# Kernel tuning notes

Measured on AMD Instinct MI355X. Metric: run time of the kernel, lower is better.

The kernel has to match this reference:

```python
import jax, jax.numpy as jnp
import numpy as np

B, N, C = 8, 2049, 768
H, NB = 12, 4
HD = C // H          # 64
SPB = (N - 1) // NB  # 512
SCALE = HD ** -0.5
EPS = 1e-6


def layer_norm(x, w, b):
    mu = jnp.mean(x, axis=-1, keepdims=True)
    var = jnp.mean((x - mu) ** 2, axis=-1, keepdims=True)
    return (x - mu) * jax.lax.rsqrt(var + EPS) * w + b


def setup_inputs() -> dict:
    key = jax.random.key(0)
    ks = jax.random.split(key, 6)
    s = lambda fan_in: 1.0 / np.sqrt(fan_in)
    return {
        "x": jax.random.normal(ks[0], (B, N, C), jnp.float32),
        "ln1_w": jnp.ones((C,), jnp.float32),
        "ln1_b": jnp.zeros((C,), jnp.float32),
        "qkv_w": jax.random.normal(ks[1], (3 * C, C), jnp.float32) * s(C),
        "proj_w": jax.random.normal(ks[2], (C, C), jnp.float32) * s(C),
        "proj_b": jnp.zeros((C,), jnp.float32),
        "ln2_w": jnp.ones((C,), jnp.float32),
        "ln2_b": jnp.zeros((C,), jnp.float32),
        "fc1_w": jax.random.normal(ks[3], (4 * C, C), jnp.float32) * s(C),
        "fc1_b": jnp.zeros((4 * C,), jnp.float32),
        "fc2_w": jax.random.normal(ks[4], (C, 4 * C), jnp.float32) * s(4 * C),
        "fc2_b": jnp.zeros((C,), jnp.float32),
    }


def _sdpa(q, k, v):
    # q:[...,Q,D] k,v:[...,K,D]
    scores = jnp.einsum("...qd,...kd->...qk", q, k) * SCALE
    return jnp.einsum("...qk,...kd->...qd", jax.nn.softmax(scores, axis=-1), v)


def _attention(h, qkv_w, proj_w, proj_b):
    # h: [B,N,C] (already layer-normed)
    qkv = (h @ qkv_w.T).reshape(B, N, 3, H, HD).transpose(2, 0, 3, 1, 4)  # [3,B,H,N,HD]
    q, k, v = qkv[0], qkv[1], qkv[2]

    # cls token attends globally over all N keys
    cls_att = _sdpa(q[:, :, 0:1, :], k, v)            # [B,H,1,HD]
    cls = cls_att.reshape(B, 1, C) + h[:, 0:1, :]      # benign reshape (seq=1)

    qkv_c = (cls @ qkv_w.T).reshape(B, 1, 3, H, HD).transpose(2, 0, 3, 1, 4)  # [3,B,H,1,HD]
    qc, kc, vc = qkv_c[0], qkv_c[1], qkv_c[2]

    # per-branch local attention with shared cls kv prepended
    def branch(t, tc):
        tb = t[:, :, 1:, :].reshape(B, H, NB, SPB, HD)
        tcb = jnp.broadcast_to(tc[:, :, None, :, :], (B, H, NB, 1, HD))
        return jnp.concatenate([tcb, tb], axis=3)      # [B,H,NB,SPB+1,HD]

    out = _sdpa(branch(q, qc), branch(k, kc), branch(v, vc))[:, :, :, 1:, :]  # [B,H,NB,SPB,HD]
    # faithful replication of the source's reshape((B, spb, C)) on a [B,H,spb,HD]
    # tensor WITHOUT head transpose (raw row-major reinterpretation):
    out = out.transpose(0, 2, 1, 3, 4).reshape(B, NB, SPB, C).reshape(B, NB * SPB, C)

    y = jnp.concatenate([cls, out], axis=1)            # [B,N,C]
    return y @ proj_w.T + proj_b


def reference(x, ln1_w, ln1_b, qkv_w, proj_w, proj_b, ln2_w, ln2_b, fc1_w, fc1_b, fc2_w, fc2_b):
    x = x + _attention(layer_norm(x, ln1_w, ln1_b), qkv_w, proj_w, proj_b)
    h = layer_norm(x, ln2_w, ln2_b)
    h = jax.nn.gelu(h @ fc1_w.T + fc1_b, approximate=False) @ fc2_w.T + fc2_b
    return x + h
```

## Files before the change

kernel.cpp:

```cpp
#include <hip/hip_runtime.h>
#include <hip/hip_bf16.h>

typedef unsigned short u16;
typedef __attribute__((ext_vector_type(8))) short s16x8;
typedef __attribute__((ext_vector_type(4))) float f32x4;

#define MFMA16 __builtin_amdgcn_mfma_f32_16x16x32_bf16
#define AS1 __attribute__((address_space(1)))
#define AS3 __attribute__((address_space(3)))

__device__ __forceinline__ u16 f2bf(float f) {
    union { __hip_bfloat16 h; u16 u; } cv;
    cv.h = __float2bfloat16(f);
    return cv.u;
}
__device__ __forceinline__ float bf2f(u16 u) {
    unsigned int v = ((unsigned int)u) << 16;
    return __uint_as_float(v);
}
__device__ __forceinline__ void gll16(const u16* g, u16* l) {
    __builtin_amdgcn_global_load_lds((AS1 void*)g, (AS3 void*)l, 16, 0, 0);
}

__global__ void cvt_kernel(const float* __restrict__ src, u16* __restrict__ dst, int n) {
    int i = (blockIdx.x * 256 + threadIdx.x) * 4;
    if (i + 3 < n) {
        float4 v = *(const float4*)&src[i];
        u16 o0 = f2bf(v.x), o1 = f2bf(v.y), o2 = f2bf(v.z), o3 = f2bf(v.w);
        ushort4 o; o.x = o0; o.y = o1; o.z = o2; o.w = o3;
        *(ushort4*)&dst[i] = o;
    }
}

__global__ __launch_bounds__(256) void ln_kernel(const float* __restrict__ x,
                                                 const float* __restrict__ w,
                                                 const float* __restrict__ b,
                                                 u16* __restrict__ out) {
    int tok = blockIdx.x;
    int tid = threadIdx.x;
    const float* xr = x + (size_t)tok * 768;
    float v0 = xr[tid], v1 = xr[tid + 256], v2 = xr[tid + 512];
    float s = v0 + v1 + v2;
    float s2 = v0 * v0 + v1 * v1 + v2 * v2;
    #pragma unroll
    for (int d = 1; d < 64; d <<= 1) { s += __shfl_xor(s, d); s2 += __shfl_xor(s2, d); }
    __shared__ float red[8];
    int wv = tid >> 6, l = tid & 63;
    if (l == 0) { red[wv] = s; red[4 + wv] = s2; }
    __syncthreads();
    s = red[0] + red[1] + red[2] + red[3];
    s2 = red[4] + red[5] + red[6] + red[7];
    float mu = s * (1.0f / 768.0f);
    float var = s2 * (1.0f / 768.0f) - mu * mu;
    float rs = rsqrtf(var + 1e-6f);
    u16* orow = out + (size_t)tok * 768;
    orow[tid]       = f2bf((v0 - mu) * rs * w[tid]       + b[tid]);
    orow[tid + 256] = f2bf((v1 - mu) * rs * w[tid + 256] + b[tid + 256]);
    orow[tid + 512] = f2bf((v2 - mu) * rs * w[tid + 512] + b[tid + 512]);
}

template<int EPI>
__global__ __launch_bounds__(256, 2) void gemm_bt(const u16* __restrict__ A,
                                                  const u16* __restrict__ Bw,
                                                  const float* __restrict__ bias,
                                                  const float* __restrict__ res,
                                                  float* __restrict__ outF,
                                                  u16* __restrict__ outU,
                                                  int M, int N, int K) {
    __shared__ u16 lds[8192];
    const int tid = threadIdx.x;
    const int l = tid & 63, w = tid >> 6;
    const int wm = w >> 1, wn = w & 1;
    const int g = l >> 4, c = l & 15;
    const int m0 = blockIdx.y * 128, n0 = blockIdx.x * 128;

    f32x4 zf = {0.f, 0.f, 0.f, 0.f};
    f32x4 acc[4][4];
    #pragma unroll
    for (int m = 0; m < 4; ++m)
        #pragma unroll
        for (int n = 0; n < 4; ++n) acc[m][n] = zf;

    const u16* aS[2]; const u16* bS[2];
    #pragma unroll
    for (int iss = 0; iss < 2; ++iss) {
        int fs = iss * 256 + tid;
        int r = fs >> 2;
        int gk = (fs & 3) ^ ((r >> 1) & 3);
        int ra = m0 + r; if (ra > M - 1) ra = M - 1;
        aS[iss] = A + (size_t)ra * K + gk * 8;
        bS[iss] = Bw + (size_t)(n0 + r) * K + gk * 8;
    }
    u16* aD0 = &lds[(0   + w * 64) * 8];
    u16* aD1 = &lds[(256 + w * 64) * 8];
    u16* bD0 = &lds[4096 + (0   + w * 64) * 8];
    u16* bD1 = &lds[4096 + (256 + w * 64) * 8];

    int aoff[4], boff[4];
    #pragma unroll
    for (int m = 0; m < 4; ++m) {
        int r = wm * 64 + m * 16 + c;
        aoff[m] = r * 32 + ((g ^ ((r >> 1) & 3)) * 8);
        int rb = wn * 64 + m * 16 + c;
        boff[m] = 4096 + rb * 32 + ((g ^ ((rb >> 1) & 3)) * 8);
    }

    for (int k0 = 0; k0 < K; k0 += 32) {
        gll16(aS[0] + k0, aD0);
        gll16(aS[1] + k0, aD1);
        gll16(bS[0] + k0, bD0);
        gll16(bS[1] + k0, bD1);
        __syncthreads();
        s16x8 af[4], bfr[4];
        #pragma unroll
        for (int m = 0; m < 4; ++m) af[m] = *(const s16x8*)&lds[aoff[m]];
        #pragma unroll
        for (int n = 0; n < 4; ++n) bfr[n] = *(const s16x8*)&lds[boff[n]];
        #pragma unroll
        for (int m = 0; m < 4; ++m)
            #pragma unroll
            for (int n = 0; n < 4; ++n)
                acc[m][n] = MFMA16(af[m], bfr[n], acc[m][n], 0, 0, 0);
        __syncthreads();
    }

    #pragma unroll
    for (int n = 0; n < 4; ++n) {
        int col = n0 + wn * 64 + n * 16 + c;
        float bv = (EPI >= 1) ? bias[col] : 0.0f;
        #pragma unroll
        for (int m = 0; m < 4; ++m) {
            int rowb = m0 + wm * 64 + m * 16 + g * 4;
            #pragma unroll
            for (int j = 0; j < 4; ++j) {
                int row = rowb + j;
                if (row < M) {
                    float v = acc[m][n][j];
                    size_t idx = (size_t)row * N + col;
                    if (EPI == 0) {
                        outU[idx] = f2bf(v);
                    } else if (EPI == 1) {
                        outF[idx] = res[idx] + v + bv;
                    } else {
                        float t = v + bv;
                        t = 0.5f * t * (1.0f + erff(t * 0.70710678118654752f));
                        outU[idx] = f2bf(t);
                    }
                }
            }
        }
    }
}

__global__ __launch_bounds__(256) void cls_part(const u16* __restrict__ qkv,
                                                float* __restrict__ part) {
    int bid = blockIdx.x;
    int ch = bid % 17;
    int hh = (bid / 17) % 12;
    int b = bid / (17 * 12);
    int tid = threadIdx.x, l = tid & 63, w = tid >> 6;
    size_t base = (size_t)b * 2049 * 2304;
    float qv = bf2f(qkv[base + hh * 64 + l]);
    __shared__ float sc[128];
    __shared__ float red[8];
    __shared__ float pv[4][64];
    int j0 = ch * 128;
    int nk = 2049 - j0; if (nk > 128) nk = 128;

    for (int jj = w; jj < nk; jj += 4) {
        float kv = bf2f(qkv[base + (size_t)(j0 + jj) * 2304 + 768 + hh * 64 + l]);
        float p = qv * kv;
        p += __shfl_xor(p, 1);  p += __shfl_xor(p, 2);  p += __shfl_xor(p, 4);
        p += __shfl_xor(p, 8);  p += __shfl_xor(p, 16); p += __shfl_xor(p, 32);
        if (l == 0) sc[jj] = p * 0.125f;
    }
    __syncthreads();
    float mx = -1e30f;
    for (int jj = tid; jj < nk; jj += 256) mx = fmaxf(mx, sc[jj]);
    #pragma unroll
    for (int d = 1; d < 64; d <<= 1) mx = fmaxf(mx, __shfl_xor(mx, d));
    if (l == 0) red[w] = mx;
    __syncthreads();
    mx = fmaxf(fmaxf(red[0], red[1]), fmaxf(red[2], red[3]));
    float sum = 0.0f;
    for (int jj = tid; jj < nk; jj += 256) {
        float p = __expf(sc[jj] - mx);
        sc[jj] = p;
        sum += p;
    }
    #pragma unroll
    for (int d = 1; d < 64; d <<= 1) sum += __shfl_xor(sum, d);
    if (l == 0) red[4 + w] = sum;
    __syncthreads();
    sum = red[4] + red[5] + red[6] + red[7];

    float acc = 0.0f;
    for (int jj = w; jj < nk; jj += 4)
        acc += sc[jj] * bf2f(qkv[base + (size_t)(j0 + jj) * 2304 + 1536 + hh * 64 + l]);
    pv[w][l] = acc;
    __syncthreads();
    if (tid < 64) {
        float o = pv[0][tid] + pv[1][tid] + pv[2][tid] + pv[3][tid];
        float* rec = part + ((size_t)(b * 12 + hh) * 17 + ch) * 66;
        rec[2 + tid] = o;
        if (tid == 0) { rec[0] = mx; rec[1] = sum; }
    }
}

__global__ __launch_bounds__(64) void cls_red(const float* __restrict__ part,
                                              const u16* __restrict__ h1,
                                              u16* __restrict__ y) {
    int bid = blockIdx.x;
    int hh = bid % 12, b = bid / 12;
    int l = threadIdx.x;
    const float* recs = part + (size_t)bid * 17 * 66;
    float M = -1e30f;
    #pragma unroll
    for (int i = 0; i < 17; ++i) M = fmaxf(M, recs[i * 66]);
    float den = 0.0f, o = 0.0f;
    #pragma unroll
    for (int i = 0; i < 17; ++i) {
        float scl = __expf(recs[i * 66] - M);
        den += scl * recs[i * 66 + 1];
        o += scl * recs[i * 66 + 2 + l];
    }
    o /= den;
    float r = bf2f(h1[(size_t)b * 2049 * 768 + hh * 64 + l]);
    y[(size_t)b * 1573632 + hh * 64 + l] = f2bf(o + r);
}

__global__ __launch_bounds__(256) void qkvc_gemm(const u16* __restrict__ y,
                                                 const u16* __restrict__ wq,
                                                 u16* __restrict__ qkvc) {
    int tid = threadIdx.x, l = tid & 63, w = tid >> 6;
    int oi = blockIdx.x * 4 + w;
    int b = oi / 2304, n = oi % 2304;
    float acc = 0.0f;
    #pragma unroll
    for (int i = 0; i < 12; ++i) {
        int k = i * 64 + l;
        acc += bf2f(y[(size_t)b * 1573632 + k]) * bf2f(wq[(size_t)n * 768 + k]);
    }
    #pragma unroll
    for (int d = 1; d < 64; d <<= 1) acc += __shfl_xor(acc, d);
    if (l == 0) qkvc[b * 2304 + n] = f2bf(acc);
}

__global__ __launch_bounds__(256, 2) void battn(const u16* __restrict__ qkv,
                                                const u16* __restrict__ qkvc,
                                                u16* __restrict__ y) {
    __shared__ u16 Vt[64 * 40];
    __shared__ u16 Pl[4][32 * 40];
    int bid = blockIdx.x;
    int quarter = bid & 3, nb = (bid >> 2) & 3, h = (bid >> 4) % 12, b = bid / 192;
    int tid = threadIdx.x, l = tid & 63, w = tid >> 6, g = l >> 4, c = l & 15;
    int qbase = quarter * 128 + w * 32;
    size_t tokbase = (size_t)b * 2049 + 1 + (size_t)nb * 512;

    s16x8 qf[2][2];
    #pragma unroll
    for (int qm = 0; qm < 2; ++qm)
        #pragma unroll
        for (int kc = 0; kc < 2; ++kc)
            qf[qm][kc] = *(const s16x8*)&qkv[(tokbase + qbase + qm * 16 + c) * 2304 + h * 64 + kc * 32 + g * 8];

    f32x4 zf = {0.f, 0.f, 0.f, 0.f};
    f32x4 o[2][4];
    float mst[2][4], lst[2][4];
    #pragma unroll
    for (int qm = 0; qm < 2; ++qm) {
        #pragma unroll
        for (int dn = 0; dn < 4; ++dn) o[qm][dn] = zf;
        #pragma unroll
        for (int j = 0; j < 4; ++j) { mst[qm][j] = -1e30f; lst[qm][j] = 0.0f; }
    }

    for (int t = 0; t <= 16; ++t) {
        __syncthreads();
        if (t < 16) {
            int key = tid & 31, dg = tid >> 5;
            s16x8 vv = *(const s16x8*)&qkv[(tokbase + t * 32 + key) * 2304 + 1536 + h * 64 + dg * 8];
            #pragma unroll
            for (int i = 0; i < 8; ++i) Vt[(dg * 8 + i) * 40 + key] = (u16)vv[i];
        } else {
            for (int i = tid; i < 2560; i += 256) Vt[i] = 0;
            __syncthreads();
            if (tid < 64) Vt[tid * 40] = qkvc[b * 2304 + 1536 + h * 64 + tid];
        }
        __syncthreads();

        f32x4 sfr[2][2];
        #pragma unroll
        for (int qm = 0; qm < 2; ++qm) { sfr[qm][0] = zf; sfr[qm][1] = zf; }

        if (t < 16) {
            #pragma unroll
            for (int kn = 0; kn < 2; ++kn)
                #pragma unroll
                for (int kc = 0; kc < 2; ++kc) {
                    s16x8 bk = *(const s16x8*)&qkv[(tokbase + t * 32 + kn * 16 + c) * 2304 + 768 + h * 64 + kc * 32 + g * 8];
                    #pragma unroll
                    for (int qm = 0; qm < 2; ++qm)
                        sfr[qm][kn] = MFMA16(qf[qm][kc], bk, sfr[qm][kn], 0, 0, 0);
                }
        } else {
            #pragma unroll
            for (int kc = 0; kc < 2; ++kc) {
                s16x8 bk = {0, 0, 0, 0, 0, 0, 0, 0};
                if (c == 0) bk = *(const s16x8*)&qkvc[b * 2304 + 768 + h * 64 + kc * 32 + g * 8];
                #pragma unroll
                for (int qm = 0; qm < 2; ++qm)
                    sfr[qm][0] = MFMA16(qf[qm][kc], bk, sfr[qm][0], 0, 0, 0);
            }
        }

        #pragma unroll
        for (int qm = 0; qm < 2; ++qm) {
            #pragma unroll
            for (int j = 0; j < 4; ++j) {
                float v0 = sfr[qm][0][j] * 0.125f;
                float v1 = (t < 16) ? sfr[qm][1][j] * 0.125f : -1e30f;
                if (t == 16 && c != 0) v0 = -1e30f;
                float tm = fmaxf(v0, v1);
                tm = fmaxf(tm, __shfl_xor(tm, 1));
                tm = fmaxf(tm, __shfl_xor(tm, 2));
                tm = fmaxf(tm, __shfl_xor(tm, 4));
                tm = fmaxf(tm, __shfl_xor(tm, 8));
                float mo = mst[qm][j];
                float mn = fmaxf(mo, tm);
                float scl = __expf(mo - mn);
                float p0 = __expf(v0 - mn);
                float p1 = __expf(v1 - mn);
                float ps = p0 + p1;
                ps += __shfl_xor(ps, 1); ps += __shfl_xor(ps, 2);
                ps += __shfl_xor(ps, 4); ps += __shfl_xor(ps, 8);
                lst[qm][j] = lst[qm][j] * scl + ps;
                mst[qm][j] = mn;
                #pragma unroll
                for (int dn = 0; dn < 4; ++dn) o[qm][dn][j] *= scl;
                int q = qm * 16 + g * 4 + j;
                Pl[w][q * 40 + c] = f2bf(p0);
                Pl[w][q * 40 + 16 + c] = f2bf(p1);
            }
        }

        s16x8 pa[2], vb[4];
        #pragma unroll
        for (int qm = 0; qm < 2; ++qm) pa[qm] = *(const s16x8*)&Pl[w][(qm * 16 + c) * 40 + g * 8];
        #pragma unroll
        for (int dn = 0; dn < 4; ++dn) vb[dn] = *(const s16x8*)&Vt[(dn * 16 + c) * 40 + g * 8];
        #pragma unroll
        for (int qm = 0; qm < 2; ++qm)
            #pragma unroll
            for (int dn = 0; dn < 4; ++dn)
                o[qm][dn] = MFMA16(pa[qm], vb[dn], o[qm][dn], 0, 0, 0);
    }

    size_t ybase = (size_t)b * 1573632 + 768 + (size_t)nb * 393216 + (size_t)h * 32768;
    #pragma unroll
    for (int qm = 0; qm < 2; ++qm)
        #pragma unroll
        for (int dn = 0; dn < 4; ++dn)
            #pragma unroll
            for (int j = 0; j < 4; ++j) {
                int q = qbase + qm * 16 + g * 4 + j;
                int d = dn * 16 + c;
                y[ybase + (size_t)q * 64 + d] = f2bf(o[qm][dn][j] / lst[qm][j]);
            }
}

extern "C" void kernel_launch(void* const* d_in, const int* in_sizes, int n_in,
                              void* d_out, int out_size, void* d_ws, size_t ws_size,
                              hipStream_t stream) {
    const float* x      = (const float*)d_in[0];
    const float* ln1_w  = (const float*)d_in[1];
    const float* ln1_b  = (const float*)d_in[2];
    const float* qkv_w  = (const float*)d_in[3];
    const float* proj_w = (const float*)d_in[4];
    const float* proj_b = (const float*)d_in[5];
    const float* ln2_w  = (const float*)d_in[6];
    const float* ln2_b  = (const float*)d_in[7];
    const float* fc1_w  = (const float*)d_in[8];
    const float* fc1_b  = (const float*)d_in[9];
    const float* fc2_w  = (const float*)d_in[10];
    const float* fc2_b  = (const float*)d_in[11];
    float* out = (float*)d_out;
    char* ws = (char*)d_ws;

    u16* Wq   = (u16*)(ws + 0);
    u16* Wp   = (u16*)(ws + 3538944);
    u16* Wf1  = (u16*)(ws + 4718592);
    u16* Wf2  = (u16*)(ws + 9437184);
    u16* h1   = (u16*)(ws + 14155776);
    u16* qkv  = (u16*)(ws + 39333888);
    u16* yb   = (u16*)(ws + 114868224);
    float* x2 = (float*)(ws + 140046336);
    u16* h2   = (u16*)(ws + 190402560);
    u16* qkvc = (u16*)(ws + 215580672);
    u16* gbuf = (u16*)(ws + 14155776);
    float* part = (float*)(ws + 140046336);

    cvt_kernel<<<1728, 256, 0, stream>>>(qkv_w, Wq, 1769472);
    cvt_kernel<<<576,  256, 0, stream>>>(proj_w, Wp, 589824);
    cvt_kernel<<<2304, 256, 0, stream>>>(fc1_w, Wf1, 2359296);
    cvt_kernel<<<2304, 256, 0, stream>>>(fc2_w, Wf2, 2359296);

    ln_kernel<<<16392, 256, 0, stream>>>(x, ln1_w, ln1_b, h1);
    gemm_bt<0><<<dim3(18, 129), 256, 0, stream>>>(h1, Wq, nullptr, nullptr, nullptr, qkv, 16392, 2304, 768);
    cls_part<<<1632, 256, 0, stream>>>(qkv, part);
    cls_red<<<96, 64, 0, stream>>>(part, h1, yb);
    qkvc_gemm<<<4608, 256, 0, stream>>>(yb, Wq, qkvc);
    battn<<<1536, 256, 0, stream>>>(qkv, qkvc, yb);
    gemm_bt<1><<<dim3(6, 129), 256, 0, stream>>>(yb, Wp, proj_b, x, x2, nullptr, 16392, 768, 768);
    ln_kernel<<<16392, 256, 0, stream>>>(x2, ln2_w, ln2_b, h2);
    gemm_bt<2><<<dim3(24, 129), 256, 0, stream>>>(h2, Wf1, fc1_b, nullptr, nullptr, gbuf, 16392, 3072, 768);
    gemm_bt<1><<<dim3(6, 129), 256, 0, stream>>>(gbuf, Wf2, fc2_b, x2, out, nullptr, 16392, 768, 3072);
}
```

Baseline: 788.2 us.

## Load GEMM fragments directly from global memory and vectorize epilogue stores via LDS

The GEMM main loop stops staging A/B tiles in shared memory with global_load_lds and barriers. Each wave now reads its MFMA fragments straight from global memory, relying on the caches for reuse between waves. Occupancy is raised to 3 blocks per CU. The bf16 epilogues now stage results in a padded per-wave LDS buffer so they can be written as 16-byte row stores, and the erf GELU is replaced by a sigmoid/tanh-style approximation using fast exp and rcp. This removes the barriers and scattered 2-byte stores, but the operand loads are poorly coalesced and unpipelined, and the GELU result drifts slightly from exact erf.

```diff
diff --git a/kernel.cpp b/kernel.cpp
--- a/kernel.cpp
+++ b/kernel.cpp
@@ -6,8 +6,6 @@
 typedef __attribute__((ext_vector_type(4))) float f32x4;
 
 #define MFMA16 __builtin_amdgcn_mfma_f32_16x16x32_bf16
-#define AS1 __attribute__((address_space(1)))
-#define AS3 __attribute__((address_space(3)))
 
 __device__ __forceinline__ u16 f2bf(float f) {
     union { __hip_bfloat16 h; u16 u; } cv;
@@ -17,9 +15,6 @@
 __device__ __forceinline__ float bf2f(u16 u) {
     unsigned int v = ((unsigned int)u) << 16;
     return __uint_as_float(v);
-}
-__device__ __forceinline__ void gll16(const u16* g, u16* l) {
-    __builtin_amdgcn_global_load_lds((AS1 void*)g, (AS3 void*)l, 16, 0, 0);
 }
 
 __global__ void cvt_kernel(const float* __restrict__ src, u16* __restrict__ dst, int n) {
@@ -60,14 +55,14 @@
 }
 
 template<int EPI>
-__global__ __launch_bounds__(256, 2) void gemm_bt(const u16* __restrict__ A,
+__global__ __launch_bounds__(256, 3) void gemm_bt(const u16* __restrict__ A,
                                                   const u16* __restrict__ Bw,
                                                   const float* __restrict__ bias,
                                                   const float* __restrict__ res,
                                                   float* __restrict__ outF,
                                                   u16* __restrict__ outU,
                                                   int M, int N, int K) {
-    __shared__ u16 lds[8192];
+    __shared__ u16 cb[4][64 * 72];
     const int tid = threadIdx.x;
     const int l = tid & 63, w = tid >> 6;
     const int wm = w >> 1, wn = w & 1;
@@ -81,73 +76,73 @@
         #pragma unroll
         for (int n = 0; n < 4; ++n) acc[m][n] = zf;
 
-    const u16* aS[2]; const u16* bS[2];
-    #pragma unroll
-    for (int iss = 0; iss < 2; ++iss) {
-        int fs = iss * 256 + tid;
-        int r = fs >> 2;
-        int gk = (fs & 3) ^ ((r >> 1) & 3);
-        int ra = m0 + r; if (ra > M - 1) ra = M - 1;
-        aS[iss] = A + (size_t)ra * K + gk * 8;
-        bS[iss] = Bw + (size_t)(n0 + r) * K + gk * 8;
-    }
-    u16* aD0 = &lds[(0   + w * 64) * 8];
-    u16* aD1 = &lds[(256 + w * 64) * 8];
-    u16* bD0 = &lds[4096 + (0   + w * 64) * 8];
-    u16* bD1 = &lds[4096 + (256 + w * 64) * 8];
-
-    int aoff[4], boff[4];
+    const u16* aPtr[4]; const u16* bPtr[4];
     #pragma unroll
     for (int m = 0; m < 4; ++m) {
-        int r = wm * 64 + m * 16 + c;
-        aoff[m] = r * 32 + ((g ^ ((r >> 1) & 3)) * 8);
-        int rb = wn * 64 + m * 16 + c;
-        boff[m] = 4096 + rb * 32 + ((g ^ ((rb >> 1) & 3)) * 8);
-    }
-
+        int ra = m0 + wm * 64 + m * 16 + c; if (ra > M - 1) ra = M - 1;
+        aPtr[m] = A + (size_t)ra * K + g * 8;
+    }
+    #pragma unroll
+    for (int n = 0; n < 4; ++n)
+        bPtr[n] = Bw + (size_t)(n0 + wn * 64 + n * 16 + c) * K + g * 8;
+
+    #pragma unroll 1
     for (int k0 = 0; k0 < K; k0 += 32) {
-        gll16(aS[0] + k0, aD0);
-        gll16(aS[1] + k0, aD1);
-        gll16(bS[0] + k0, bD0);
-        gll16(bS[1] + k0, bD1);
-        __syncthreads();
-        s16x8 af[4], bfr[4];
-        #pragma unroll
-        for (int m = 0; m < 4; ++m) af[m] = *(const s16x8*)&lds[aoff[m]];
-        #pragma unroll
-        for (int n = 0; n < 4; ++n) bfr[n] = *(const s16x8*)&lds[boff[n]];
+        s16x8 af[4], bf[4];
+        #pragma unroll
+        for (int m = 0; m < 4; ++m) af[m] = *(const s16x8*)(aPtr[m] + k0);
+        #pragma unroll
+        for (int n = 0; n < 4; ++n) bf[n] = *(const s16x8*)(bPtr[n] + k0);
         #pragma unroll
         for (int m = 0; m < 4; ++m)
             #pragma unroll
             for (int n = 0; n < 4; ++n)
-                acc[m][n] = MFMA16(af[m], bfr[n], acc[m][n], 0, 0, 0);
-        __syncthreads();
-    }
-
-    #pragma unroll
-    for (int n = 0; n < 4; ++n) {
-        int col = n0 + wn * 64 + n * 16 + c;
-        float bv = (EPI >= 1) ? bias[col] : 0.0f;
-        #pragma unroll
-        for (int m = 0; m < 4; ++m) {
-            int rowb = m0 + wm * 64 + m * 16 + g * 4;
-            #pragma unroll
-            for (int j = 0; j < 4; ++j) {
-                int row = rowb + j;
-                if (row < M) {
-                    float v = acc[m][n][j];
-                    size_t idx = (size_t)row * N + col;
-                    if (EPI == 0) {
-                        outU[idx] = f2bf(v);
-                    } else if (EPI == 1) {
-                        outF[idx] = res[idx] + v + bv;
-                    } else {
-                        float t = v + bv;
-                        t = 0.5f * t * (1.0f + erff(t * 0.70710678118654752f));
-                        outU[idx] = f2bf(t);
+                acc[m][n] = MFMA16(af[m], bf[n], acc[m][n], 0, 0, 0);
+    }
+
+    if (EPI == 1) {
+        #pragma unroll
+        for (int n = 0; n < 4; ++n) {
+            int col = n0 + wn * 64 + n * 16 + c;
+            float bv = bias[col];
+            #pragma unroll
+            for (int m = 0; m < 4; ++m) {
+                int rowb = m0 + wm * 64 + m * 16 + g * 4;
+                #pragma unroll
+                for (int j = 0; j < 4; ++j) {
+                    int row = rowb + j;
+                    if (row < M) {
+                        size_t idx = (size_t)row * N + col;
+                        outF[idx] = res[idx] + acc[m][n][j] + bv;
                     }
                 }
             }
+        }
+    } else {
+        #pragma unroll
+        for (int n = 0; n < 4; ++n) {
+            float bv = (EPI == 2) ? bias[n0 + wn * 64 + n * 16 + c] : 0.0f;
+            #pragma unroll
+            for (int m = 0; m < 4; ++m)
+                #pragma unroll
+                for (int j = 0; j < 4; ++j) {
+                    float v = acc[m][n][j];
+                    if (EPI == 2) {
+                        float tt = v + bv;
+                        float sg = __expf(-(1.59576912f * tt + 0.0713548162f * tt * tt * tt));
+                        v = tt * __builtin_amdgcn_rcpf(1.0f + sg);
+                    }
+                    cb[w][(m * 16 + g * 4 + j) * 72 + n * 16 + c] = f2bf(v);
+                }
+        }
+        #pragma unroll
+        for (int it = 0; it < 8; ++it) {
+            int r = it * 8 + (l >> 3);
+            int cg = (l & 7) * 8;
+            s16x8 v = *(const s16x8*)&cb[w][r * 72 + cg];
+            int grow = m0 + wm * 64 + r;
+            if (grow < M)
+                *(s16x8*)&outU[(size_t)grow * N + n0 + wn * 64 + cg] = v;
         }
     }
 }
```

Measured after the change: 1.288 ms. 1.63x slower.
